# Performance work log

Hardware: AMD Instinct MI355X
Metric: run time of the kernel (lower is better)

## Reference

```python
import jax, jax.numpy as jnp
import numpy as np

N, E, T = 20000, 320000, 4
F_IN, HID, F_OUT = 128, 256, 128
EPS = 1e-5  # torch BatchNorm1d default


def _gcn_layer(x, src, dst, ew, W, b, gamma, beta):
    # gather-scale-scatter: out[dst] += ew_e * x[src]
    msgs = ew[:, :, None] * x[src]                      # (E, T, F)
    agg = jax.ops.segment_sum(msgs, dst, num_segments=N)  # (N, T, F)
    h = jnp.einsum('ntf,fh->nth', agg, W) + b            # (N, T, H)
    # BatchNorm1d over channel dim H (training-mode batch stats over N and T)
    mean = h.mean(axis=(0, 1))
    var = h.var(axis=(0, 1))
    h = (h - mean) * jax.lax.rsqrt(var + EPS) * gamma + beta
    return jax.nn.relu(h)


def setup_inputs() -> dict:
    key = jax.random.key(0)
    ks = jax.random.split(key, 8)
    node_features = jax.random.normal(ks[0], (N, T, F_IN), jnp.float32)
    edge_index = jax.random.randint(ks[1], (2, E), 0, N, dtype=jnp.int32)
    edges_weight = jax.random.uniform(ks[2], (E, T), jnp.float32)
    s0 = 1.0 / np.sqrt(F_IN)
    s1 = 1.0 / np.sqrt(HID)
    W0 = jax.random.uniform(ks[3], (F_IN, HID), jnp.float32, -s0, s0)
    b0 = jax.random.uniform(ks[4], (HID,), jnp.float32, -s0, s0)
    W1 = jax.random.uniform(ks[5], (HID, F_OUT), jnp.float32, -s1, s1)
    b1 = jax.random.uniform(ks[6], (F_OUT,), jnp.float32, -s1, s1)
    g0 = jnp.ones((HID,), jnp.float32)
    be0 = jnp.zeros((HID,), jnp.float32)
    g1 = jnp.ones((F_OUT,), jnp.float32)
    be1 = jnp.zeros((F_OUT,), jnp.float32)
    return {"node_features": node_features, "edge_index": edge_index,
            "edges_weight": edges_weight, "W0": W0, "b0": b0, "g0": g0,
            "be0": be0, "W1": W1, "b1": b1, "g1": g1, "be1": be1}


def reference(node_features, edge_index, edges_weight,
              W0, b0, g0, be0, W1, b1, g1, be1):
    src, dst = edge_index[0], edge_index[1]
    h = _gcn_layer(node_features, src, dst, edges_weight, W0, b0, g0, be0)
    h = _gcn_layer(h, src, dst, edges_weight, W1, b1, g1, be1)
    return h
```

## Files before the change

### kernel.cpp

```cpp
#include <hip/hip_runtime.h>


#define T_DIM 4
#define F_DIM 128
#define HID   256
#define TF    512

typedef __attribute__((ext_vector_type(8))) short bf16x8;
typedef __attribute__((ext_vector_type(4))) float f32x4;

__device__ __forceinline__ ushort f2bf(float x) {
    union { float f; unsigned u; } v; v.f = x;
    unsigned r = v.u + 0x7FFF + ((v.u >> 16) & 1);
    return (ushort)(r >> 16);
}
__device__ __forceinline__ float bf2f(ushort b) {
    union { float f; unsigned u; } v; v.u = ((unsigned)b) << 16;
    return v.f;
}
__device__ __forceinline__ void gl_lds16(const void* gsrc, void* ldst) {
    __builtin_amdgcn_global_load_lds(
        (const __attribute__((address_space(1))) unsigned*)gsrc,
        (__attribute__((address_space(3))) unsigned*)ldst, 16, 0, 0);
}

__global__ void count_kernel(const int* __restrict__ dst, int E, int* __restrict__ deg) {
    int e = blockIdx.x * blockDim.x + threadIdx.x;
    if (e < E) atomicAdd(&deg[dst[e]], 1);
}

__global__ void scan_kernel(const int* __restrict__ deg, int* __restrict__ row_start,
                            int* __restrict__ cursor, int n) {
    __shared__ int part[1024];
    int tid = threadIdx.x;
    int chunk = (n + 1023) >> 10;
    int begin = tid * chunk; if (begin > n) begin = n;
    int end = begin + chunk; if (end > n) end = n;
    int s = 0;
    for (int i = begin; i < end; ++i) s += deg[i];
    part[tid] = s;
    __syncthreads();
    for (int off = 1; off < 1024; off <<= 1) {
        int v = (tid >= off) ? part[tid - off] : 0;
        __syncthreads();
        part[tid] += v;
        __syncthreads();
    }
    int excl = (tid == 0) ? 0 : part[tid - 1];
    for (int i = begin; i < end; ++i) {
        row_start[i] = excl; cursor[i] = excl; excl += deg[i];
    }
    if (tid == 1023) row_start[n] = part[1023];
}

__global__ void fill_kernel(const int* __restrict__ src, const int* __restrict__ dst,
                            const float4* __restrict__ ew, int E,
                            int* __restrict__ cursor, int* __restrict__ esrc,
                            float4* __restrict__ ewr) {
    int e = blockIdx.x * blockDim.x + threadIdx.x;
    if (e < E) {
        int d = dst[e];
        int p = atomicAdd(&cursor[d], 1);
        esrc[p] = src[e];
        ewr[p] = ew[e];
    }
}

__global__ void wsplit_kernel(const float* __restrict__ W, int K, int NC,
                              ushort* __restrict__ hi, ushort* __restrict__ lo) {
    int idx = blockIdx.x * 256 + threadIdx.x;
    if (idx >= K * NC) return;
    int k = idx / NC, c = idx % NC;
    float x = W[idx];
    ushort h = f2bf(x);
    hi[(size_t)c * K + k] = h;
    lo[(size_t)c * K + k] = f2bf(x - bf2f(h));
}

template<bool BF16OUT>
__global__ __launch_bounds__(256) void agg_kernel(
        const float4* __restrict__ x4, const float* __restrict__ ewr,
        const int* __restrict__ row_start, const int* __restrict__ esrc,
        float4* __restrict__ out4, ushort* __restrict__ ohi, ushort* __restrict__ olo) {
    const int n = blockIdx.x;
    const int tid = threadIdx.x;
    const int p = tid >> 6;
    const int q = tid & 63;
    const int t = q >> 4;
    const int beg = row_start[n], end = row_start[n + 1];
    float4 accA = make_float4(0.f, 0.f, 0.f, 0.f);
    float4 accB = make_float4(0.f, 0.f, 0.f, 0.f);
    for (int i = beg; i < end; i += 4) {
        const int e = i + p;
        if (e < end) {
            const int s = esrc[e];
            const float4* xr = x4 + (size_t)s * 128;
            const float w = ewr[e * 4 + t];
            float4 va = xr[2 * q], vb = xr[2 * q + 1];
            accA.x = fmaf(w, va.x, accA.x); accA.y = fmaf(w, va.y, accA.y);
            accA.z = fmaf(w, va.z, accA.z); accA.w = fmaf(w, va.w, accA.w);
            accB.x = fmaf(w, vb.x, accB.x); accB.y = fmaf(w, vb.y, accB.y);
            accB.z = fmaf(w, vb.z, accB.z); accB.w = fmaf(w, vb.w, accB.w);
        }
    }
    __shared__ float4 red[3][128];
    if (p) { red[p - 1][2 * q] = accA; red[p - 1][2 * q + 1] = accB; }
    __syncthreads();
    if (p == 0) {
        #pragma unroll
        for (int r = 0; r < 3; ++r) {
            float4 a = red[r][2 * q], b = red[r][2 * q + 1];
            accA.x += a.x; accA.y += a.y; accA.z += a.z; accA.w += a.w;
            accB.x += b.x; accB.y += b.y; accB.z += b.z; accB.w += b.w;
        }
        if (BF16OUT) {
            float v[8] = {accA.x, accA.y, accA.z, accA.w, accB.x, accB.y, accB.z, accB.w};
            uint4 hw, lw;
            unsigned hu[4], lu[4];
            #pragma unroll
            for (int j = 0; j < 4; ++j) {
                ushort h0 = f2bf(v[2 * j]), h1 = f2bf(v[2 * j + 1]);
                ushort l0 = f2bf(v[2 * j] - bf2f(h0)), l1 = f2bf(v[2 * j + 1] - bf2f(h1));
                hu[j] = (unsigned)h0 | ((unsigned)h1 << 16);
                lu[j] = (unsigned)l0 | ((unsigned)l1 << 16);
            }
            hw.x = hu[0]; hw.y = hu[1]; hw.z = hu[2]; hw.w = hu[3];
            lw.x = lu[0]; lw.y = lu[1]; lw.z = lu[2]; lw.w = lu[3];
            *(uint4*)&ohi[(size_t)n * TF + q * 8] = hw;
            *(uint4*)&olo[(size_t)n * TF + q * 8] = lw;
        } else {
            out4[(size_t)n * 128 + 2 * q] = accA;
            out4[(size_t)n * 128 + 2 * q + 1] = accB;
        }
    }
}

template<int BM, int K, int NC, bool FUSE>
__global__ __launch_bounds__(256, 4) void gemm_mfma(
        const ushort* __restrict__ A_hi, const ushort* __restrict__ A_lo,
        const float* __restrict__ Af32,
        const ushort* __restrict__ Wt_hi, const ushort* __restrict__ Wt_lo,
        const float* __restrict__ scale, const float* __restrict__ shift,
        float* __restrict__ out) {
    constexpr int BN = 128;
    constexpr int MT = BM / 64;
    __shared__ __align__(16) unsigned char AsH[BM * 64], AsL[BM * 64];
    __shared__ __align__(16) unsigned char WsH[BN * 64], WsL[BN * 64];
    const int tid = threadIdx.x;
    const int w = tid >> 6, l = tid & 63;
    const long rowbase = (long)blockIdx.y * BM;
    const int colbase = blockIdx.x * BN;

    f32x4 acc[MT][8];
    #pragma unroll
    for (int mt = 0; mt < MT; ++mt)
        #pragma unroll
        for (int nt = 0; nt < 8; ++nt) acc[mt][nt] = (f32x4){0.f, 0.f, 0.f, 0.f};

    for (int kb = 0; kb < K / 32; ++kb) {
        if (kb) __syncthreads();
        {
            const int b = l & 3;
            #pragma unroll
            for (int cc = 0; cc < 2; ++cc) {
                int c = 2 * w + cc;
                int cl = c * 16 + (l >> 2);
                size_t go = (size_t)(colbase + cl) * K + kb * 32 + ((b ^ (cl & 3)) << 3);
                gl_lds16(Wt_hi + go, WsH + c * 1024);
                gl_lds16(Wt_lo + go, WsL + c * 1024);
            }
        }
        if (!FUSE) {
            const int b = l & 3;
            #pragma unroll
            for (int cc = 0; cc < BM / 64; ++cc) {
                int c = w * (BM / 64) + cc;
                int r = c * 16 + (l >> 2);
                size_t go = (size_t)(rowbase + r) * K + kb * 32 + ((b ^ (r & 3)) << 3);
                gl_lds16(A_hi + go, AsH + c * 1024);
                gl_lds16(A_lo + go, AsL + c * 1024);
            }
        } else {
            #pragma unroll
            for (int p = 0; p < BM * 32 / 1024; ++p) {
                int idx = p * 256 + tid;
                int r = idx >> 3, k4 = idx & 7;
                float4 v = *(const float4*)&Af32[(rowbase + r) * K + kb * 32 + k4 * 4];
                int ch = kb * 32 + k4 * 4;
                float4 sc = *(const float4*)&scale[ch];
                float4 sh = *(const float4*)&shift[ch];
                v.x = fmaxf(fmaf(sc.x, v.x, sh.x), 0.f);
                v.y = fmaxf(fmaf(sc.y, v.y, sh.y), 0.f);
                v.z = fmaxf(fmaf(sc.z, v.z, sh.z), 0.f);
                v.w = fmaxf(fmaf(sc.w, v.w, sh.w), 0.f);
                ushort h[4], lo[4];
                float vv[4] = {v.x, v.y, v.z, v.w};
                #pragma unroll
                for (int j = 0; j < 4; ++j) {
                    h[j] = f2bf(vv[j]);
                    lo[j] = f2bf(vv[j] - bf2f(h[j]));
                }
                unsigned long long hq = (unsigned long long)((unsigned)h[0] | ((unsigned)h[1] << 16))
                                      | ((unsigned long long)((unsigned)h[2] | ((unsigned)h[3] << 16)) << 32);
                unsigned long long lq = (unsigned long long)((unsigned)lo[0] | ((unsigned)lo[1] << 16))
                                      | ((unsigned long long)((unsigned)lo[2] | ((unsigned)lo[3] << 16)) << 32);
                int off = r * 64 + (((k4 >> 1) ^ (r & 3)) << 4) + (k4 & 1) * 8;
                *(unsigned long long*)(AsH + off) = hq;
                *(unsigned long long*)(AsL + off) = lq;
            }
        }
        __syncthreads();

        const int g = l >> 4;
        bf16x8 ah[MT], al[MT];
        #pragma unroll
        for (int mt = 0; mt < MT; ++mt) {
            int ar = w * 16 * MT + mt * 16 + (l & 15);
            int off = ar * 64 + ((g ^ (ar & 3)) << 4);
            ah[mt] = *(const bf16x8*)(AsH + off);
            al[mt] = *(const bf16x8*)(AsL + off);
        }
        #pragma unroll
        for (int nt = 0; nt < 8; ++nt) {
            int bc = nt * 16 + (l & 15);
            int off = bc * 64 + ((g ^ (bc & 3)) << 4);
            bf16x8 bh = *(const bf16x8*)(WsH + off);
            bf16x8 bl = *(const bf16x8*)(WsL + off);
            #pragma unroll
            for (int mt = 0; mt < MT; ++mt) {
                acc[mt][nt] = __builtin_amdgcn_mfma_f32_16x16x32_bf16(ah[mt], bh, acc[mt][nt], 0, 0, 0);
                acc[mt][nt] = __builtin_amdgcn_mfma_f32_16x16x32_bf16(ah[mt], bl, acc[mt][nt], 0, 0, 0);
                acc[mt][nt] = __builtin_amdgcn_mfma_f32_16x16x32_bf16(al[mt], bh, acc[mt][nt], 0, 0, 0);
            }
        }
    }

    #pragma unroll
    for (int mt = 0; mt < MT; ++mt) {
        long r0 = rowbase + w * 16 * MT + mt * 16 + (l >> 4) * 4;
        #pragma unroll
        for (int nt = 0; nt < 8; ++nt) {
            int c = colbase + nt * 16 + (l & 15);
            #pragma unroll
            for (int j = 0; j < 4; ++j)
                out[(size_t)(r0 + j) * NC + c] = acc[mt][nt][j];
        }
    }
}

template<int C>
__global__ __launch_bounds__(256) void stats_kernel(
        const float* __restrict__ h, int rows,
        float* __restrict__ sums, float* __restrict__ sqs) {
    constexpr int Q = C / 4;
    constexpr int RPB = 256 / Q;
    const int q = threadIdx.x & (Q - 1);
    const int sub = threadIdx.x / Q;
    float4 s = make_float4(0.f, 0.f, 0.f, 0.f);
    float4 s2 = make_float4(0.f, 0.f, 0.f, 0.f);
    for (long r = (long)blockIdx.x * RPB + sub; r < rows; r += (long)gridDim.x * RPB) {
        float4 v = *(const float4*)&h[r * C + q * 4];
        s.x += v.x; s.y += v.y; s.z += v.z; s.w += v.w;
        s2.x = fmaf(v.x, v.x, s2.x); s2.y = fmaf(v.y, v.y, s2.y);
        s2.z = fmaf(v.z, v.z, s2.z); s2.w = fmaf(v.w, v.w, s2.w);
    }
    __shared__ float4 redS[256], redQ[256];
    redS[threadIdx.x] = s; redQ[threadIdx.x] = s2;
    __syncthreads();
    if (sub == 0) {
        #pragma unroll
        for (int u = 1; u < RPB; ++u) {
            float4 a = redS[u * Q + q], b = redQ[u * Q + q];
            s.x += a.x; s.y += a.y; s.z += a.z; s.w += a.w;
            s2.x += b.x; s2.y += b.y; s2.z += b.z; s2.w += b.w;
        }
        atomicAdd(&sums[q * 4 + 0], s.x); atomicAdd(&sums[q * 4 + 1], s.y);
        atomicAdd(&sums[q * 4 + 2], s.z); atomicAdd(&sums[q * 4 + 3], s.w);
        atomicAdd(&sqs[q * 4 + 0], s2.x); atomicAdd(&sqs[q * 4 + 1], s2.y);
        atomicAdd(&sqs[q * 4 + 2], s2.z); atomicAdd(&sqs[q * 4 + 3], s2.w);
    }
}

__global__ void finalize_kernel(const float* __restrict__ sums, const float* __restrict__ sqs,
                                const float* __restrict__ g, const float* __restrict__ be,
                                float* __restrict__ scale, float* __restrict__ shift,
                                int C, float invR) {
    int c = threadIdx.x;
    if (c < C) {
        float mean = sums[c] * invR;
        float var = sqs[c] * invR - mean * mean;
        float a = g[c] * rsqrtf(var + 1e-5f);
        scale[c] = a;
        shift[c] = fmaf(-mean, a, be[c]);
    }
}

__global__ void bnapply_kernel(const float4* __restrict__ h4,
                               const float* __restrict__ scale, const float* __restrict__ shift,
                               float4* __restrict__ out4, int n4) {
    int i = blockIdx.x * 256 + threadIdx.x;
    if (i >= n4) return;
    float4 v = h4[i];
    int cb = (i & 31) << 2;
    float4 sc = *(const float4*)&scale[cb];
    float4 sh = *(const float4*)&shift[cb];
    v.x = fmaxf(fmaf(sc.x, v.x, sh.x), 0.f);
    v.y = fmaxf(fmaf(sc.y, v.y, sh.y), 0.f);
    v.z = fmaxf(fmaf(sc.z, v.z, sh.z), 0.f);
    v.w = fmaxf(fmaf(sc.w, v.w, sh.w), 0.f);
    out4[i] = v;
}

extern "C" void kernel_launch(void* const* d_in, const int* in_sizes, int n_in,
                              void* d_out, int out_size, void* d_ws, size_t ws_size,
                              hipStream_t stream) {
    const float* x   = (const float*)d_in[0];
    const int*   ei  = (const int*)d_in[1];
    const float* ew  = (const float*)d_in[2];
    const float* W0  = (const float*)d_in[3];
    const float* g0  = (const float*)d_in[5];
    const float* be0 = (const float*)d_in[6];
    const float* W1  = (const float*)d_in[7];
    const float* g1  = (const float*)d_in[9];
    const float* be1 = (const float*)d_in[10];
    float* out = (float*)d_out;

    const int N = in_sizes[0] / TF;
    const int E = in_sizes[1] / 2;
    const int ROWS = N * T_DIM;

    const int* src = ei;
    const int* dst = ei + E;

    float* h1  = (float*)d_ws;
    float* y2  = h1 + (size_t)ROWS * HID;
    float* h2  = y2 + (size_t)ROWS * F_DIM;
    ushort* A1h = (ushort*)h2;
    ushort* A1l = A1h + (size_t)ROWS * F_DIM;
    int* deg       = (int*)(h2 + (size_t)ROWS * F_DIM);
    int* row_start = deg + N;
    int* cursor    = row_start + N + 1;
    int* esrc      = cursor + N + 3;
    float* ewr     = (float*)(esrc + E);
    float* sums0   = ewr + (size_t)E * 4;
    float* sqs0    = sums0 + HID;
    float* sums1   = sqs0 + HID;
    float* sqs1    = sums1 + F_DIM;
    float* scale0  = sqs1 + F_DIM;
    float* shift0  = scale0 + HID;
    float* scale1  = shift0 + HID;
    float* shift1  = scale1 + F_DIM;
    ushort* Wt0h   = (ushort*)(shift1 + F_DIM);
    ushort* Wt0l   = Wt0h + 256 * 128;
    ushort* Wt1h   = Wt0l + 256 * 128;
    ushort* Wt1l   = Wt1h + 128 * 256;

    hipMemsetAsync(deg, 0, N * sizeof(int), stream);
    hipMemsetAsync(sums0, 0, (2 * HID + 2 * F_DIM) * sizeof(float), stream);

    const int eb = (E + 255) / 256;
    count_kernel<<<eb, 256, 0, stream>>>(dst, E, deg);
    scan_kernel<<<1, 1024, 0, stream>>>(deg, row_start, cursor, N);
    fill_kernel<<<eb, 256, 0, stream>>>(src, dst, (const float4*)ew, E, cursor,
                                        esrc, (float4*)ewr);
    wsplit_kernel<<<128, 256, 0, stream>>>(W0, 128, 256, Wt0h, Wt0l);
    wsplit_kernel<<<128, 256, 0, stream>>>(W1, 256, 128, Wt1h, Wt1l);

    agg_kernel<true><<<N, 256, 0, stream>>>((const float4*)x, ewr, row_start, esrc,
                                            nullptr, A1h, A1l);
    gemm_mfma<128, 128, 256, false><<<dim3(2, ROWS / 128), 256, 0, stream>>>(
        A1h, A1l, nullptr, Wt0h, Wt0l, nullptr, nullptr, h1);
    stats_kernel<256><<<256, 256, 0, stream>>>(h1, ROWS, sums0, sqs0);
    finalize_kernel<<<1, 256, 0, stream>>>(sums0, sqs0, g0, be0, scale0, shift0, HID,
                                           1.f / (float)ROWS);

    gemm_mfma<64, 256, 128, true><<<dim3(1, ROWS / 64), 256, 0, stream>>>(
        nullptr, nullptr, h1, Wt1h, Wt1l, scale0, shift0, y2);
    agg_kernel<false><<<N, 256, 0, stream>>>((const float4*)y2, ewr, row_start, esrc,
                                             (float4*)h2, nullptr, nullptr);
    stats_kernel<128><<<256, 256, 0, stream>>>(h2, ROWS, sums1, sqs1);
    finalize_kernel<<<1, 128, 0, stream>>>(sums1, sqs1, g1, be1, scale1, shift1, F_DIM,
                                           1.f / (float)ROWS);
    bnapply_kernel<<<(ROWS * F_DIM / 4 + 255) / 256, 256, 0, stream>>>(
        (const float4*)h2, scale1, shift1, (float4*)out, ROWS * F_DIM / 4);
}
```

Baseline: 536.5 us.

## Fuse BatchNorm statistics into GEMM and aggregation epilogues; unroll edge gather loop

Removes both standalone stats kernels by having the first GEMM accumulate per-channel sums and squared sums from its accumulators, and having the second aggregation kernel do the same from its reduced outputs. Shared-memory atomics combine values within a block, followed by one global atomic per channel per block. The aggregation loop now handles four edges per wave per iteration with separate accumulators, so more independent gathers are in flight. The cost is many more global atomics (one set per node block in the aggregation), extra LDS atomics, and higher register pressure.

```diff
diff --git a/kernel.cpp b/kernel.cpp
--- a/kernel.cpp
+++ b/kernel.cpp
@@ -77,33 +77,63 @@
     lo[(size_t)c * K + k] = f2bf(x - bf2f(h));
 }
 
-template<bool BF16OUT>
+template<bool BF16OUT, bool DOSTATS>
 __global__ __launch_bounds__(256) void agg_kernel(
         const float4* __restrict__ x4, const float* __restrict__ ewr,
         const int* __restrict__ row_start, const int* __restrict__ esrc,
-        float4* __restrict__ out4, ushort* __restrict__ ohi, ushort* __restrict__ olo) {
+        float4* __restrict__ out4, ushort* __restrict__ ohi, ushort* __restrict__ olo,
+        float* __restrict__ sums, float* __restrict__ sqs) {
     const int n = blockIdx.x;
     const int tid = threadIdx.x;
     const int p = tid >> 6;
     const int q = tid & 63;
     const int t = q >> 4;
     const int beg = row_start[n], end = row_start[n + 1];
-    float4 accA = make_float4(0.f, 0.f, 0.f, 0.f);
-    float4 accB = make_float4(0.f, 0.f, 0.f, 0.f);
-    for (int i = beg; i < end; i += 4) {
-        const int e = i + p;
-        if (e < end) {
-            const int s = esrc[e];
-            const float4* xr = x4 + (size_t)s * 128;
-            const float w = ewr[e * 4 + t];
-            float4 va = xr[2 * q], vb = xr[2 * q + 1];
-            accA.x = fmaf(w, va.x, accA.x); accA.y = fmaf(w, va.y, accA.y);
-            accA.z = fmaf(w, va.z, accA.z); accA.w = fmaf(w, va.w, accA.w);
-            accB.x = fmaf(w, vb.x, accB.x); accB.y = fmaf(w, vb.y, accB.y);
-            accB.z = fmaf(w, vb.z, accB.z); accB.w = fmaf(w, vb.w, accB.w);
-        }
-    }
+
+    float4 aA[4], aB[4];
+    #pragma unroll
+    for (int st = 0; st < 4; ++st) {
+        aA[st] = make_float4(0.f, 0.f, 0.f, 0.f);
+        aB[st] = make_float4(0.f, 0.f, 0.f, 0.f);
+    }
+    const int last = end - 1;
+    for (int i = beg; i < end; i += 16) {
+        int sIdx[4]; float wv[4];
+        #pragma unroll
+        for (int st = 0; st < 4; ++st) {
+            int e = i + 4 * st + p;
+            int ec = (e < end) ? e : last;
+            sIdx[st] = esrc[ec];
+            wv[st] = (e < end) ? ewr[ec * 4 + t] : 0.f;
+        }
+        float4 va[4], vb[4];
+        #pragma unroll
+        for (int st = 0; st < 4; ++st) {
+            const float4* xr = x4 + (size_t)sIdx[st] * 128 + 2 * q;
+            va[st] = xr[0];
+            vb[st] = xr[1];
+        }
+        #pragma unroll
+        for (int st = 0; st < 4; ++st) {
+            const float w = wv[st];
+            aA[st].x = fmaf(w, va[st].x, aA[st].x); aA[st].y = fmaf(w, va[st].y, aA[st].y);
+            aA[st].z = fmaf(w, va[st].z, aA[st].z); aA[st].w = fmaf(w, va[st].w, aA[st].w);
+            aB[st].x = fmaf(w, vb[st].x, aB[st].x); aB[st].y = fmaf(w, vb[st].y, aB[st].y);
+            aB[st].z = fmaf(w, vb[st].z, aB[st].z); aB[st].w = fmaf(w, vb[st].w, aB[st].w);
+        }
+    }
+    float4 accA = make_float4(aA[0].x + aA[1].x + aA[2].x + aA[3].x,
+                              aA[0].y + aA[1].y + aA[2].y + aA[3].y,
+                              aA[0].z + aA[1].z + aA[2].z + aA[3].z,
+                              aA[0].w + aA[1].w + aA[2].w + aA[3].w);
+    float4 accB = make_float4(aB[0].x + aB[1].x + aB[2].x + aB[3].x,
+                              aB[0].y + aB[1].y + aB[2].y + aB[3].y,
+                              aB[0].z + aB[1].z + aB[2].z + aB[3].z,
+                              aB[0].w + aB[1].w + aB[2].w + aB[3].w);
+
     __shared__ float4 red[3][128];
+    __shared__ float chS[128], chQ[128];
+    if (DOSTATS && tid < 128) { chS[tid] = 0.f; chQ[tid] = 0.f; }
     if (p) { red[p - 1][2 * q] = accA; red[p - 1][2 * q + 1] = accB; }
     __syncthreads();
     if (p == 0) {
@@ -132,24 +162,43 @@
             out4[(size_t)n * 128 + 2 * q] = accA;
             out4[(size_t)n * 128 + 2 * q + 1] = accB;
         }
-    }
-}
-
-template<int BM, int K, int NC, bool FUSE>
+        if (DOSTATS) {
+            float v[8] = {accA.x, accA.y, accA.z, accA.w, accB.x, accB.y, accB.z, accB.w};
+            #pragma unroll
+            for (int u = 0; u < 8; ++u) {
+                int ch = (q * 8 + u) & 127;
+                atomicAdd(&chS[ch], v[u]);
+                atomicAdd(&chQ[ch], v[u] * v[u]);
+            }
+        }
+    }
+    if (DOSTATS) {
+        __syncthreads();
+        if (tid < 128) {
+            atomicAdd(&sums[tid], chS[tid]);
+            atomicAdd(&sqs[tid], chQ[tid]);
+        }
+    }
+}
+
+template<int BM, int K, int NC, bool FUSE, bool DOSTATS>
 __global__ __launch_bounds__(256, 4) void gemm_mfma(
         const ushort* __restrict__ A_hi, const ushort* __restrict__ A_lo,
         const float* __restrict__ Af32,
         const ushort* __restrict__ Wt_hi, const ushort* __restrict__ Wt_lo,
         const float* __restrict__ scale, const float* __restrict__ shift,
-        float* __restrict__ out) {
+        float* __restrict__ out, float* __restrict__ sums, float* __restrict__ sqs) {
     constexpr int BN = 128;
     constexpr int MT = BM / 64;
     __shared__ __align__(16) unsigned char AsH[BM * 64], AsL[BM * 64];
     __shared__ __align__(16) unsigned char WsH[BN * 64], WsL[BN * 64];
+    __shared__ float chS[128], chQ[128];
     const int tid = threadIdx.x;
     const int w = tid >> 6, l = tid & 63;
     const long rowbase = (long)blockIdx.y * BM;
     const int colbase = blockIdx.x * BN;
+
+    if (DOSTATS && tid < 128) { chS[tid] = 0.f; chQ[tid] = 0.f; }
 
     f32x4 acc[MT][8];
     #pragma unroll
@@ -182,8 +231,8 @@
             }
         } else {
             #pragma unroll
-            for (int p = 0; p < BM * 32 / 1024; ++p) {
-                int idx = p * 256 + tid;
+            for (int pp = 0; pp < BM * 32 / 1024; ++pp) {
+                int idx = pp * 256 + tid;
                 int r = idx >> 3, k4 = idx & 7;
                 float4 v = *(const float4*)&Af32[(rowbase + r) * K + kb * 32 + k4 * 4];
                 int ch = kb * 32 + k4 * 4;
@@ -246,38 +295,27 @@
                 out[(size_t)(r0 + j) * NC + c] = acc[mt][nt][j];
         }
     }
-}
-
-template<int C>
-__global__ __launch_bounds__(256) void stats_kernel(
-        const float* __restrict__ h, int rows,
-        float* __restrict__ sums, float* __restrict__ sqs) {
-    constexpr int Q = C / 4;
-    constexpr int RPB = 256 / Q;
-    const int q = threadIdx.x & (Q - 1);
-    const int sub = threadIdx.x / Q;
-    float4 s = make_float4(0.f, 0.f, 0.f, 0.f);
-    float4 s2 = make_float4(0.f, 0.f, 0.f, 0.f);
-    for (long r = (long)blockIdx.x * RPB + sub; r < rows; r += (long)gridDim.x * RPB) {
-        float4 v = *(const float4*)&h[r * C + q * 4];
-        s.x += v.x; s.y += v.y; s.z += v.z; s.w += v.w;
-        s2.x = fmaf(v.x, v.x, s2.x); s2.y = fmaf(v.y, v.y, s2.y);
-        s2.z = fmaf(v.z, v.z, s2.z); s2.w = fmaf(v.w, v.w, s2.w);
-    }
-    __shared__ float4 redS[256], redQ[256];
-    redS[threadIdx.x] = s; redQ[threadIdx.x] = s2;
-    __syncthreads();
-    if (sub == 0) {
-        #pragma unroll
-        for (int u = 1; u < RPB; ++u) {
-            float4 a = redS[u * Q + q], b = redQ[u * Q + q];
-            s.x += a.x; s.y += a.y; s.z += a.z; s.w += a.w;
-            s2.x += b.x; s2.y += b.y; s2.z += b.z; s2.w += b.w;
-        }
-        atomicAdd(&sums[q * 4 + 0], s.x); atomicAdd(&sums[q * 4 + 1], s.y);
-        atomicAdd(&sums[q * 4 + 2], s.z); atomicAdd(&sums[q * 4 + 3], s.w);
-        atomicAdd(&sqs[q * 4 + 0], s2.x); atomicAdd(&sqs[q * 4 + 1], s2.y);
-        atomicAdd(&sqs[q * 4 + 2], s2.z); atomicAdd(&sqs[q * 4 + 3], s2.w);
+    if (DOSTATS) {
+        #pragma unroll
+        for (int nt = 0; nt < 8; ++nt) {
+            float s = 0.f, qq = 0.f;
+            #pragma unroll
+            for (int mt = 0; mt < MT; ++mt)
+                #pragma unroll
+                for (int j = 0; j < 4; ++j) {
+                    float v = acc[mt][nt][j];
+                    s += v;
+                    qq = fmaf(v, v, qq);
+                }
+            int ch = nt * 16 + (l & 15);
+            atomicAdd(&chS[ch], s);
+            atomicAdd(&chQ[ch], qq);
+        }
+        __syncthreads();
+        if (tid < 128) {
+            atomicAdd(&sums[colbase + tid], chS[tid]);
+            atomicAdd(&sqs[colbase + tid], chQ[tid]);
+        }
     }
 }
 
@@ -366,19 +404,19 @@
     wsplit_kernel<<<128, 256, 0, stream>>>(W0, 128, 256, Wt0h, Wt0l);
     wsplit_kernel<<<128, 256, 0, stream>>>(W1, 256, 128, Wt1h, Wt1l);
 
-    agg_kernel<true><<<N, 256, 0, stream>>>((const float4*)x, ewr, row_start, esrc,
-                                            nullptr, A1h, A1l);
-    gemm_mfma<128, 128, 256, false><<<dim3(2, ROWS / 128), 256, 0, stream>>>(
-        A1h, A1l, nullptr, Wt0h, Wt0l, nullptr, nullptr, h1);
-    stats_kernel<256><<<256, 256, 0, stream>>>(h1, ROWS, sums0, sqs0);
+    agg_kernel<true, false><<<N, 256, 0, stream>>>((const float4*)x, ewr, row_start,
+                                                   esrc, nullptr, A1h, A1l,
+                                                   nullptr, nullptr);
+    gemm_mfma<128, 128, 256, false, true><<<dim3(2, ROWS / 128), 256, 0, stream>>>(
+        A1h, A1l, nullptr, Wt0h, Wt0l, nullptr, nullptr, h1, sums0, sqs0);
     finalize_kernel<<<1, 256, 0, stream>>>(sums0, sqs0, g0, be0, scale0, shift0, HID,
                                            1.f / (float)ROWS);
 
-    gemm_mfma<64, 256, 128, true><<<dim3(1, ROWS / 64), 256, 0, stream>>>(
-        nullptr, nullptr, h1, Wt1h, Wt1l, scale0, shift0, y2);
-    agg_kernel<false><<<N, 256, 0, stream>>>((const float4*)y2, ewr, row_start, esrc,
-                                             (float4*)h2, nullptr, nullptr);
-    stats_kernel<128><<<256, 256, 0, stream>>>(h2, ROWS, sums1, sqs1);
+    gemm_mfma<64, 256, 128, true, false><<<dim3(1, ROWS / 64), 256, 0, stream>>>(
+        nullptr, nullptr, h1, Wt1h, Wt1l, scale0, shift0, y2, nullptr, nullptr);
+    agg_kernel<false, true><<<N, 256, 0, stream>>>((const float4*)y2, ewr, row_start,
+                                                   esrc, (float4*)h2, nullptr, nullptr,
+                                                   sums1, sqs1);
     finalize_kernel<<<1, 128, 0, stream>>>(sums1, sqs1, g1, be1, scale1, shift1, F_DIM,
                                            1.f / (float)ROWS);
     bnapply_kernel<<<(ROWS * F_DIM / 4 + 255) / 256, 256, 0, stream>>>(
```

New measurement: 1.031 ms. 92.1% more time.
